# Optimization experiments

Hardware: AMD Instinct MI355X
Metric: run time of the kernel (lower is better)

## Reference

```python
import jax, jax.numpy as jnp
import numpy as np

N, K = 256, 133
INPUT_W, INPUT_H = 256, 256
SPLIT = 2.0
W = round(INPUT_W * SPLIT)  # 512
H = round(INPUT_H * SPLIT)  # 512
SIGMA = (5.66, 5.66)
BETA = 10.0
LABEL_BETA = 10.0


def setup_inputs() -> dict:
    key = jax.random.key(0)
    k1, k2, k3 = jax.random.split(key, 3)
    pred = jax.random.normal(k1, (N, K, W + H), dtype=jnp.float32)
    xy = jax.random.uniform(k2, (N, K, 2), dtype=jnp.float32) * INPUT_W
    vis = (jax.random.uniform(k3, (N, K, 1), dtype=jnp.float32) > 0.2).astype(jnp.float32)
    keypoints = jnp.concatenate([xy, vis], axis=-1)
    return {"pred": pred, "keypoints": keypoints}


def _gaussian_targets(keypoints):
    # Vectorized equivalent of the Python (n,k) loop in gaussian_smoothng.
    kp_xy = keypoints[..., :2]
    vis = keypoints[..., 2]
    mu = jnp.round(kp_xy * SPLIT)  # int64 in torch; rounded float is numerically identical
    rx = SIGMA[0] * 3.0
    ry = SIGMA[1] * 3.0
    left = mu[..., 0] - rx
    right = mu[..., 0] + rx + 1.0
    top = mu[..., 1] - ry
    bottom = mu[..., 1] + ry + 1.0
    oob = (left >= W) | (top >= H) | (right < 0) | (bottom < 0)
    visible = vis >= 0.5
    valid = visible & (~oob)
    x = jnp.arange(W, dtype=jnp.float32)
    y = jnp.arange(H, dtype=jnp.float32)
    gx = jnp.exp(-((x[None, None, :] - mu[..., 0:1]) ** 2) / (2.0 * SIGMA[0] ** 2))
    gy = jnp.exp(-((y[None, None, :] - mu[..., 1:2]) ** 2) / (2.0 * SIGMA[1] ** 2))
    target_x = jnp.where(valid[..., None], gx, 0.0)  # (N,K,W)
    target_y = jnp.where(valid[..., None], gy, 0.0)  # (N,K,H)
    # weight = visible value, zeroed if visible but out of bounds
    weight = jnp.where(visible & oob, 0.0, vis)
    return target_x, target_y, weight


def _criterion(p, t):
    # p, t: (N*K, L). KLDivLoss(reduction='none') then mean over dim=1.
    log_pt = jax.nn.log_softmax(p * BETA, axis=1)
    lab = jax.nn.softmax(t * LABEL_BETA, axis=1)  # strictly positive
    kl = lab * (jnp.log(lab) - log_pt)
    return kl.mean(axis=1)


def reference(pred, keypoints):
    n, k, _ = pred.shape
    split = pred.shape[-1] // 2
    pred_x = pred[..., :split].reshape(-1, split)
    pred_y = pred[..., split:].reshape(-1, pred.shape[-1] - split)
    gt_x, gt_y, w = _gaussian_targets(keypoints)
    w = w.reshape(-1)
    loss_x = (_criterion(pred_x, gt_x.reshape(-1, W)) * w).sum()
    loss_y = (_criterion(pred_y, gt_y.reshape(-1, H)) * w).sum()
    return (loss_x + loss_y) / k
```

## Files before the change

### kernel.cpp

```cpp
#include <hip/hip_runtime.h>
#include <math.h>

#define NKP 133
#define NROWS (256 * NKP)
#define RH_TOTAL (2 * NROWS)
#define NQUADS (RH_TOTAL / 4)
#define NBLOCKS 2048
#define NWAVES (NBLOCKS * 4)
#define C2P  14.4269504088896f
#define NK2  0.02251706f
#define RAD  16.98f
#define LN2f 0.69314718055994531f
#define WTAPS 5

static __device__ __forceinline__ float fexp2(float x) { return __builtin_amdgcn_exp2f(x); }
static __device__ __forceinline__ float frcp (float x) { return __builtin_amdgcn_rcpf(x); }

__global__ __launch_bounds__(256) void rtmcc_partial_kernel(
    const float* __restrict__ pred,
    const float* __restrict__ keypoints,
    float* __restrict__ partials)
{
    const int wave = threadIdx.x >> 6;
    const int lane = threadIdx.x & 63;
    const int g    = lane >> 4;
    const int l4   = lane & 15;
    const int gh   = g >> 1;
    const int h    = g & 1;
    __shared__ float2 twb[256];
    __shared__ float lds[4];

    int q = blockIdx.x * 4 + wave;

    float kx, ky, kv;
    {
        const int row = 2 * q + gh;
        kx = keypoints[row * 3 + 0];
        ky = keypoints[row * 3 + 1];
        kv = keypoints[row * 3 + 2];
    }

    {
        const int t = threadIdx.x;
        const float d = (float)(t - 128);
        float em1 = 0.0f, eg = 0.0f;
        if (fabsf(d) <= 35.0f) {
            const float gg = fexp2(-d * d * NK2);
            const float e  = fexp2(gg * C2P);
            em1 = e - 1.0f; eg = e * gg;
        }
        twb[t] = make_float2(em1, eg);
    }
    __syncthreads();

    float acc = 0.0f;

    for (; q < NQUADS; q += NWAVES) {
        const float kxc = kx, kyc = ky, kvc = kv;
        const int qn = q + NWAVES;
        if (qn < NQUADS) {
            const int rown = 2 * qn + gh;
            kx = keypoints[rown * 3 + 0];
            ky = keypoints[rown * 3 + 1];
            kv = keypoints[rown * 3 + 2];
        }

        const float mux = rintf(kxc * 2.0f);
        const float muy = rintf(kyc * 2.0f);
        const bool oob = (mux - RAD >= 512.0f) || (muy - RAD >= 512.0f) ||
                         (mux + RAD + 1.0f < 0.0f) || (muy + RAD + 1.0f < 0.0f);
        const bool visible = (kvc >= 0.5f);
        const float w = (visible && oob) ? 0.0f : kvc;
        const bool act = (w > 0.0f);

        float S = 0.0f, Zw = 0.0f, R = 0.0f;
        if (act) {
            const float* ph = pred + (size_t)(4 * q + g) * 512;

            float4 qa0, qa1, qa2, qa3, qb0, qb1, qb2, qb3;
            qa0 = *reinterpret_cast<const float4*>(ph +   0 + l4 * 4);
            qa1 = *reinterpret_cast<const float4*>(ph +  64 + l4 * 4);
            qa2 = *reinterpret_cast<const float4*>(ph + 128 + l4 * 4);
            qa3 = *reinterpret_cast<const float4*>(ph + 192 + l4 * 4);
            qb0 = *reinterpret_cast<const float4*>(ph + 256 + l4 * 4);
            qb1 = *reinterpret_cast<const float4*>(ph + 320 + l4 * 4);
            qb2 = *reinterpret_cast<const float4*>(ph + 384 + l4 * 4);
            qb3 = *reinterpret_cast<const float4*>(ph + 448 + l4 * 4);

            float s0 = 0.f, s1 = 0.f, r0 = 0.f, r1 = 0.f;
#define BULK4(Q0, Q1)                                                          \
            s0 += fexp2(C2P*Q0.x) + fexp2(C2P*Q0.y)                            \
                + fexp2(C2P*Q0.z) + fexp2(C2P*Q0.w);                           \
            r0 -= (Q0.x + Q0.y) + (Q0.z + Q0.w);                               \
            s1 += fexp2(C2P*Q1.x) + fexp2(C2P*Q1.y)                            \
                + fexp2(C2P*Q1.z) + fexp2(C2P*Q1.w);                           \
            r1 -= (Q1.x + Q1.y) + (Q1.z + Q1.w);
            BULK4(qa0, qa1)
            BULK4(qa2, qa3)
            BULK4(qb0, qb1)
            BULK4(qb2, qb3)
#undef BULK4
            S = s0 + s1; R = r0 + r1;

            const float mu = h ? muy : mux;
            const int mui = (int)mu;
            int ws = mui - 40; ws = ws < 0 ? 0 : (ws > 432 ? 432 : ws);
            #pragma unroll
            for (int v = 0; v < WTAPS; ++v) {
                const int idx = ws + l4 + v * 16;
                const float pw = ph[idx];
                const float2 te = twb[idx - mui + 128];
                Zw += te.x;
                R  += te.y - te.x * pw;
            }
        }

        #pragma unroll
        for (int off = 1; off < 16; off <<= 1) {
            S  += __shfl_xor(S,  off, 64);
            Zw += __shfl_xor(Zw, off, 64);
            R  += __shfl_xor(R,  off, 64);
        }

        if (act) {
            const float Z = 512.0f + Zw;
            acc += w * (10.0f * R * frcp(Z) + (__log2f(S) - __log2f(Z)) * LN2f);
        }
    }

    acc *= (1.0f / (16.0f * 512.0f * 133.0f));
    #pragma unroll
    for (int off = 1; off < 64; off <<= 1) acc += __shfl_xor(acc, off, 64);
    if (lane == 0) lds[wave] = acc;
    __syncthreads();
    if (threadIdx.x == 0)
        partials[blockIdx.x] = lds[0] + lds[1] + lds[2] + lds[3];
}

__global__ __launch_bounds__(64) void rtmcc_reduce_kernel(
    const float* __restrict__ partials, float* __restrict__ out)
{
    float s = 0.0f;
    #pragma unroll
    for (int i = 0; i < NBLOCKS / 64; ++i) s += partials[i * 64 + threadIdx.x];
    #pragma unroll
    for (int off = 1; off < 64; off <<= 1) s += __shfl_xor(s, off, 64);
    if (threadIdx.x == 0) out[0] = s;
}

extern "C" void kernel_launch(void* const* d_in, const int* in_sizes, int n_in,
                              void* d_out, int out_size, void* d_ws, size_t ws_size,
                              hipStream_t stream) {
    const float* pred = (const float*)d_in[0];
    const float* kpts = (const float*)d_in[1];
    float* out = (float*)d_out;
    float* partials = (float*)d_ws;

    rtmcc_partial_kernel<<<NBLOCKS, 256, 0, stream>>>(pred, kpts, partials);
    rtmcc_reduce_kernel<<<1, 64, 0, stream>>>(partials, out);
}
```

Baseline: 24.60 us.

## Split tail rows across all waves with one-row-per-wave processing

The main loop now covers only an exact multiple of the wave count's quads, so every wave runs the same number of iterations. The leftover row-halves (fewer than one full round of quads) are spread one per wave, and the whole 64-lane wave processes each of them with a different window and tap layout. This removes the partial final iteration in which only some waves did work, at the cost of a second code path and extra registers for the prefetched tail keypoint.

```diff
diff --git a/kernel.cpp b/kernel.cpp
--- a/kernel.cpp
+++ b/kernel.cpp
@@ -4,9 +4,11 @@
 #define NKP 133
 #define NROWS (256 * NKP)
 #define RH_TOTAL (2 * NROWS)
-#define NQUADS (RH_TOTAL / 4)
 #define NBLOCKS 2048
 #define NWAVES (NBLOCKS * 4)
+#define NQ_MAIN (2 * NWAVES)
+#define RH_BASE (4 * NQ_MAIN)
+#define RH_LEFT (RH_TOTAL - RH_BASE)
 #define C2P  14.4269504088896f
 #define NK2  0.02251706f
 #define RAD  16.98f
@@ -27,10 +29,11 @@
     const int l4   = lane & 15;
     const int gh   = g >> 1;
     const int h    = g & 1;
+    const int wid  = blockIdx.x * 4 + wave;
     __shared__ float2 twb[256];
     __shared__ float lds[4];
 
-    int q = blockIdx.x * 4 + wave;
+    int q = wid;
 
     float kx, ky, kv;
     {
@@ -38,6 +41,14 @@
         kx = keypoints[row * 3 + 0];
         ky = keypoints[row * 3 + 1];
         kv = keypoints[row * 3 + 2];
+    }
+    float k3x = 0.f, k3y = 0.f, k3v = 0.f;
+    const bool has3 = (wid < RH_LEFT);
+    if (has3) {
+        const int row3 = (RH_BASE + wid) >> 1;
+        k3x = keypoints[row3 * 3 + 0];
+        k3y = keypoints[row3 * 3 + 1];
+        k3v = keypoints[row3 * 3 + 2];
     }
 
     {
@@ -54,11 +65,12 @@
     __syncthreads();
 
     float acc = 0.0f;
-
-    for (; q < NQUADS; q += NWAVES) {
+    float acc3 = 0.0f;
+
+    for (; q < NQ_MAIN; q += NWAVES) {
         const float kxc = kx, kyc = ky, kvc = kv;
         const int qn = q + NWAVES;
-        if (qn < NQUADS) {
+        if (qn < NQ_MAIN) {
             const int rown = 2 * qn + gh;
             kx = keypoints[rown * 3 + 0];
             ky = keypoints[rown * 3 + 1];
@@ -128,10 +140,54 @@
         }
     }
 
-    acc *= (1.0f / (16.0f * 512.0f * 133.0f));
+    if (has3) {
+        const float mux = rintf(k3x * 2.0f);
+        const float muy = rintf(k3y * 2.0f);
+        const bool oob = (mux - RAD >= 512.0f) || (muy - RAD >= 512.0f) ||
+                         (mux + RAD + 1.0f < 0.0f) || (muy + RAD + 1.0f < 0.0f);
+        const bool visible = (k3v >= 0.5f);
+        const float w = (visible && oob) ? 0.0f : k3v;
+        if (w > 0.0f) {
+            const int rh = RH_BASE + wid;
+            const float mu = (rh & 1) ? muy : mux;
+            const float* pr = pred + (size_t)rh * 512;
+
+            const float* p = pr + lane * 8;
+            const float4 pa = *reinterpret_cast<const float4*>(p);
+            const float4 pb = *reinterpret_cast<const float4*>(p + 4);
+
+            float S = 0.f, R = 0.f;
+            S += fexp2(C2P*pa.x) + fexp2(C2P*pa.y) + fexp2(C2P*pa.z) + fexp2(C2P*pa.w);
+            S += fexp2(C2P*pb.x) + fexp2(C2P*pb.y) + fexp2(C2P*pb.z) + fexp2(C2P*pb.w);
+            R -= (pa.x + pa.y) + (pa.z + pa.w) + (pb.x + pb.y) + (pb.z + pb.w);
+
+            const int mui = (int)mu;
+            int ws = mui - 64; ws = ws < 0 ? 0 : (ws > 384 ? 384 : ws);
+            const float pw0 = pr[ws + lane];
+            const float pw1 = pr[ws + 64 + lane];
+            int t0 = ws + lane - mui + 128;
+            int t1 = t0 + 64;
+            const float2 te0 = twb[t0];
+            const float2 te1 = twb[t1];
+            float Zw = te0.x + te1.x;
+            R += (te0.y - te0.x * pw0) + (te1.y - te1.x * pw1);
+
+            #pragma unroll
+            for (int off = 1; off < 64; off <<= 1) {
+                S  += __shfl_xor(S,  off, 64);
+                Zw += __shfl_xor(Zw, off, 64);
+                R  += __shfl_xor(R,  off, 64);
+            }
+            const float Z = 512.0f + Zw;
+            acc3 = w * (10.0f * R * frcp(Z) + (__log2f(S) - __log2f(Z)) * LN2f);
+        }
+    }
+
+    float accv = acc * (1.0f / (16.0f * 512.0f * 133.0f))
+               + acc3 * (1.0f / (64.0f * 512.0f * 133.0f));
     #pragma unroll
-    for (int off = 1; off < 64; off <<= 1) acc += __shfl_xor(acc, off, 64);
-    if (lane == 0) lds[wave] = acc;
+    for (int off = 1; off < 64; off <<= 1) accv += __shfl_xor(accv, off, 64);
+    if (lane == 0) lds[wave] = accv;
     __syncthreads();
     if (threadIdx.x == 0)
         partials[blockIdx.x] = lds[0] + lds[1] + lds[2] + lds[3];
```

Result: no change. 25.01 us (+1.7%).
